# Performance work log

Measured on AMD Instinct MI355X. Metric: run time of the kernel, lower is better.

The kernel has to match this reference:

```python
import jax, jax.numpy as jnp
import numpy as np
import math

B, M, V, C, HID, BIN, H, W = 2, 1024, 300, 128, 128, 256, 384, 512


def fibonacci_sphere(n):
    # generate_grasp_views: n approximately-uniform directions on the unit sphere
    i = np.arange(n, dtype=np.float64)
    phi = (np.sqrt(5.0) - 1.0) / 2.0
    z = (2.0 * i + 1.0) / n - 1.0
    r = np.sqrt(np.maximum(1.0 - z * z, 0.0))
    t = 2.0 * np.pi * i * phi
    v = np.stack([r * np.cos(t), r * np.sin(t), z], -1)
    return (v / np.linalg.norm(v, axis=-1, keepdims=True)).astype(np.float32)


def setup_inputs():
    key = jax.random.key(0)
    ks = jax.random.split(key, 24)
    seed_features = jax.random.normal(ks[0], (B, C, M), jnp.float32)
    token_sel_idx = jax.random.randint(ks[1], (B, M), 0, H * W)
    fx = 525.0
    Kmat = jnp.array([[fx, 0.0, W / 2.0], [0.0, fx, H / 2.0], [0.0, 0.0, 1.0]], jnp.float32)
    K = jnp.broadcast_to(Kmat, (B, 3, 3))
    depth_map = 0.2 + 0.8 * jax.random.uniform(ks[2], (B, 1, H, W), jnp.float32)
    depth_prob = jax.nn.softmax(jax.random.normal(ks[3], (B, BIN, H, W), jnp.float32), axis=1)
    view_dirs = jnp.asarray(fibonacci_sphere(V))

    def lin(k, fan_in, shape):
        s = 1.0 / np.sqrt(fan_in)
        return jax.random.uniform(k, shape, jnp.float32, -s, s)

    qin = C + 7  # seed_feat + ray(3) + normal(3) + uncert(1)
    params = dict(
        Wq1=lin(ks[4], qin, (qin, HID)), bq1=lin(ks[5], qin, (HID,)),
        Wq2=lin(ks[6], HID, (HID, HID)), bq2=lin(ks[7], HID, (HID,)),
        Wa1=lin(ks[8], 3, (3, HID)), ba1=lin(ks[9], 3, (HID,)),
        Wa2=lin(ks[10], HID, (HID, HID)), ba2=lin(ks[11], HID, (HID,)),
        Wb1=lin(ks[12], 3, (3, HID // 2)), bb1=lin(ks[13], 3, (HID // 2,)),
        Wb2=lin(ks[14], HID // 2, (HID // 2, 1)), bb2=lin(ks[15], HID // 2, (1,)),
        Wr1=lin(ks[16], HID, (HID, C)), br1=lin(ks[17], HID, (C,)),
        Wr2=lin(ks[18], C, (C, C)), br2=lin(ks[19], C, (C,)),
    )
    return dict(seed_features=seed_features, token_sel_idx=token_sel_idx, K=K,
                depth_map=depth_map, depth_prob=depth_prob, view_dirs=view_dirs, **params)


def _views_to_rot(views):
    # batch_viewpoint_params_to_matrix(-views, angle=0)
    axis_x = -views
    zero = jnp.zeros_like(axis_x[..., 0])
    axis_y = jnp.stack([-axis_x[..., 1], axis_x[..., 0], zero], -1)
    ny = jnp.linalg.norm(axis_y, axis=-1, keepdims=True)
    fallback = jnp.broadcast_to(jnp.array([0.0, 1.0, 0.0], views.dtype), axis_y.shape)
    axis_y = jnp.where(ny < 1e-8, fallback, axis_y / jnp.maximum(ny, 1e-8))
    axis_x = axis_x / jnp.maximum(jnp.linalg.norm(axis_x, axis=-1, keepdims=True), 1e-8)
    axis_z = jnp.cross(axis_x, axis_y)
    return jnp.stack([axis_x, axis_y, axis_z], -1)  # (B,M,3,3)


def _forward(seed_features, token_sel_idx, K, depth_map, depth_prob, view_dirs,
             Wq1, bq1, Wq2, bq2, Wa1, ba1, Wa2, ba2, Wb1, bb1, Wb2, bb2, Wr1, br1, Wr2, br2):
    depth_map = jax.lax.stop_gradient(depth_map)   # .detach() in torch
    depth_prob = jax.lax.stop_gradient(depth_prob)
    # --- backproject depth to xyz map (B,3,H,W) ---
    ys, xs = jnp.meshgrid(jnp.arange(H, dtype=jnp.float32), jnp.arange(W, dtype=jnp.float32), indexing='ij')
    fx = K[:, 0, 0][:, None, None, None]; fy = K[:, 1, 1][:, None, None, None]
    cx = K[:, 0, 2][:, None, None, None]; cy = K[:, 1, 2][:, None, None, None]
    z = depth_map
    x = (xs[None, None] - cx) / fx * z
    y = (ys[None, None] - cy) / fy * z
    xyz = jnp.concatenate([x, y, z], axis=1)
    # --- central-difference normal map with replicate pad ---
    dx = (xyz[:, :, :, 2:] - xyz[:, :, :, :-2])[:, :, 1:-1, :]
    dy = (xyz[:, :, 2:, :] - xyz[:, :, :-2, :])[:, :, :, 1:-1]
    n = jnp.cross(dx.transpose(0, 2, 3, 1), dy.transpose(0, 2, 3, 1))
    n = n / jnp.maximum(jnp.linalg.norm(n, axis=-1, keepdims=True), 1e-6)
    normal_map = jnp.pad(n.transpose(0, 3, 1, 2), ((0, 0), (0, 0), (1, 1), (1, 1)), mode='edge')
    # --- depth uncertainty: normalized entropy over bins ---
    p = jnp.maximum(depth_prob, 1e-8)
    uncert_map = jnp.clip(-(p * jnp.log(p)).sum(axis=1, keepdims=True) / math.log(BIN), 0.0, 1.0)
    # --- per-seed irregular gathers ---
    def gather(feat, idx):
        Bf, Cf = feat.shape[0], feat.shape[1]
        flat = feat.reshape(Bf, Cf, H * W)
        return jnp.take_along_axis(flat, jnp.broadcast_to(idx[:, None, :], (Bf, Cf, idx.shape[1])), axis=2)
    normal_bm3 = gather(normal_map, token_sel_idx).transpose(0, 2, 1)  # (B,M,3)
    uncert_bm1 = gather(uncert_map, token_sel_idx).transpose(0, 2, 1)  # (B,M,1)
    u = (token_sel_idx % W).astype(jnp.float32)
    v = (token_sel_idx // W).astype(jnp.float32)
    rx = (u - K[:, 0, 2][:, None]) / K[:, 0, 0][:, None]
    ry = (v - K[:, 1, 2][:, None]) / K[:, 1, 1][:, None]
    rays = jnp.stack([rx, ry, jnp.ones_like(rx)], -1)
    rays = rays / jnp.maximum(jnp.linalg.norm(rays, axis=-1, keepdims=True), 1e-12)
    normal_bm3 = normal_bm3 * (1.0 - uncert_bm1)
    # --- query / anchor / bias MLPs ---
    q_in = jnp.concatenate([seed_features.transpose(0, 2, 1), rays, normal_bm3, uncert_bm1], -1)
    q = jax.nn.relu(jax.nn.relu(q_in @ Wq1 + bq1) @ Wq2 + bq2)          # (B,M,HID)
    a = jax.nn.relu(view_dirs @ Wa1 + ba1) @ Wa2 + ba2                  # (V,HID)
    bias = (jax.nn.relu(view_dirs @ Wb1 + bb1) @ Wb2 + bb2)[:, 0]        # (V,)
    logits = jnp.einsum('bmh,vh->bmv', q, a) / jnp.sqrt(jnp.float32(HID)) + bias
    view_score = jax.nn.sigmoid(logits)                                  # (B,M,V)
    # --- top-1 view selection + gather xyz / rot / anchor feat ---
    top_inds = jnp.argmax(view_score, axis=-1)                           # (B,M)
    top_xyz = view_dirs[top_inds]                                        # (B,M,3)
    rot = _views_to_rot(top_xyz)                                         # (B,M,3,3)
    top_a = a[top_inds]                                                  # (B,M,HID)
    res = jax.nn.relu((q + top_a) @ Wr1 + br1) @ Wr2 + br2               # (B,M,C)
    res_feat = res.transpose(0, 2, 1)                                    # (B,C,M)
    return view_score, top_inds, top_xyz, rot, res_feat


def reference(seed_features, token_sel_idx, K, depth_map, depth_prob, view_dirs,
              Wq1, bq1, Wq2, bq2, Wa1, ba1, Wa2, ba2, Wb1, bb1, Wb2, bb2, Wr1, br1, Wr2, br2):
    return _forward(seed_features, token_sel_idx, K, depth_map, depth_prob, view_dirs,
                    Wq1, bq1, Wq2, bq2, Wa1, ba1, Wa2, ba2, Wb1, bb1, Wb2, bb2, Wr1, br1, Wr2, br2)
```

## Files before the change

kernel.cpp:

```cpp
#include <hip/hip_runtime.h>
#include <math.h>

#define B 2
#define M 1024
#define V 300
#define C 128
#define HID 128
#define BIN 256
#define H 384
#define W 512
#define QIN (C + 7)
#define G 4

__global__ __launch_bounds__(HID) void anchor_kernel(
    const float* __restrict__ view_dirs,
    const float* __restrict__ Wa1, const float* __restrict__ ba1,
    const float* __restrict__ Wa2, const float* __restrict__ ba2,
    const float* __restrict__ Wb1, const float* __restrict__ bb1,
    const float* __restrict__ Wb2, const float* __restrict__ bb2,
    float* __restrict__ a_out, float* __restrict__ aT_out,
    float* __restrict__ bias_out) {
  const int v = blockIdx.x;
  const int t = threadIdx.x;
  __shared__ float h1[HID];

  const float vd0 = view_dirs[v * 3 + 0];
  const float vd1 = view_dirs[v * 3 + 1];
  const float vd2 = view_dirs[v * 3 + 2];

  float h = vd0 * Wa1[0 * HID + t] + vd1 * Wa1[1 * HID + t] + vd2 * Wa1[2 * HID + t] + ba1[t];
  h1[t] = fmaxf(h, 0.0f);

  if (t < 64) {
    float x = vd0 * Wb1[0 * 64 + t] + vd1 * Wb1[1 * 64 + t] + vd2 * Wb1[2 * 64 + t] + bb1[t];
    x = fmaxf(x, 0.0f) * Wb2[t];
#pragma unroll
    for (int o = 32; o > 0; o >>= 1) x += __shfl_down(x, o, 64);
    if (t == 0) bias_out[v] = x + bb2[0];
  }
  __syncthreads();

  float acc = ba2[t];
#pragma unroll 8
  for (int k = 0; k < HID; ++k) acc += h1[k] * Wa2[k * HID + t];
  a_out[v * HID + t] = acc;
  aT_out[(size_t)t * V + v] = acc;
}

__global__ __launch_bounds__(128) void seed_kernel(
    const float* __restrict__ seed, const int* __restrict__ token_sel_idx,
    const float* __restrict__ Kmat, const float* __restrict__ depth_map,
    const float* __restrict__ depth_prob, const float* __restrict__ view_dirs,
    const float* __restrict__ Wq1, const float* __restrict__ bq1,
    const float* __restrict__ Wq2, const float* __restrict__ bq2,
    const float* __restrict__ Wr1, const float* __restrict__ br1,
    const float* __restrict__ Wr2, const float* __restrict__ br2,
    const float* __restrict__ a_ws, const float* __restrict__ aT_ws,
    const float* __restrict__ bias_ws,
    float* __restrict__ out_view_score, float* __restrict__ out_top_inds,
    float* __restrict__ out_top_xyz, float* __restrict__ out_rot,
    float* __restrict__ out_res) {
  const int s0 = blockIdx.x * G;
  const int b = s0 >> 10;
  const int m0 = s0 & (M - 1);
  const int t = threadIdx.x;
  const int lane = t & 63;
  const int wv = t >> 6;

  __shared__ __align__(16) float qin_s[G][136];
  __shared__ __align__(16) float hs[G][HID];
  __shared__ __align__(16) float qs[G][HID];
  __shared__ __align__(16) float sum_s[G][HID];
  __shared__ float ered[G][2];
  __shared__ float wbv[G][2];
  __shared__ int   wbi[G][2];
  __shared__ int   sbest[G];
  __shared__ int   sidx[G];

  if (t < G) sidx[t] = token_sel_idx[b * M + m0 + t];

  const float4 sv = *(const float4*)&seed[((size_t)b * C + t) * M + m0];
  __syncthreads();

  float pe[2 * G];
  {
    const size_t HW = (size_t)H * W;
#pragma unroll
    for (int g = 0; g < G; ++g) {
      const float* dp = depth_prob + (size_t)b * BIN * HW + sidx[g];
      pe[2 * g + 0] = dp[(size_t)(2 * t + 0) * HW];
      pe[2 * g + 1] = dp[(size_t)(2 * t + 1) * HW];
    }
  }

  float zl = 0.f, zr = 0.f, zu = 0.f, zd = 0.f;
  int w_r = 0, h_r = 0, wc_r = 0, hc_r = 0;
  if (t < G) {
    const int idx = sidx[t];
    w_r = idx % W;
    h_r = idx / W;
    hc_r = min(max(h_r, 1), H - 2);
    wc_r = min(max(w_r, 1), W - 2);
    const float* dm = depth_map + (size_t)b * H * W;
    zl = dm[hc_r * W + (wc_r - 1)];
    zr = dm[hc_r * W + (wc_r + 1)];
    zu = dm[(hc_r - 1) * W + wc_r];
    zd = dm[(hc_r + 1) * W + wc_r];
  }

  qin_s[0][t] = sv.x; qin_s[1][t] = sv.y; qin_s[2][t] = sv.z; qin_s[3][t] = sv.w;
  if (t < G) qin_s[t][135] = 0.0f;
  __syncthreads();

  float acc[G];
  {
    const float b1 = bq1[t];
#pragma unroll
    for (int g = 0; g < G; ++g) acc[g] = b1;
    for (int i0 = 0; i0 < 128; i0 += 4) {
      const float w0 = Wq1[(i0 + 0) * HID + t];
      const float w1 = Wq1[(i0 + 1) * HID + t];
      const float w2 = Wq1[(i0 + 2) * HID + t];
      const float w3 = Wq1[(i0 + 3) * HID + t];
#pragma unroll
      for (int g = 0; g < G; ++g) {
        const float4 qv = *(const float4*)&qin_s[g][i0];
        acc[g] += qv.x * w0 + qv.y * w1 + qv.z * w2 + qv.w * w3;
      }
    }
  }

  {
    float e[G];
#pragma unroll
    for (int g = 0; g < G; ++g) {
      const float p0 = fmaxf(pe[2 * g + 0], 1e-8f);
      const float p1 = fmaxf(pe[2 * g + 1], 1e-8f);
      e[g] = p0 * logf(p0) + p1 * logf(p1);
    }
#pragma unroll
    for (int o = 32; o > 0; o >>= 1) {
#pragma unroll
      for (int g = 0; g < G; ++g) e[g] += __shfl_down(e[g], o, 64);
    }
    if (lane == 0) {
#pragma unroll
      for (int g = 0; g < G; ++g) ered[g][wv] = e[g];
    }
  }
  __syncthreads();

  if (t < G) {
    const int g = t;
    float uncert = (-(ered[g][0] + ered[g][1])) / 5.5451774444795623f;
    uncert = fminf(fmaxf(uncert, 0.0f), 1.0f);

    const float fx = Kmat[b * 9 + 0], fy = Kmat[b * 9 + 4];
    const float cx = Kmat[b * 9 + 2], cy = Kmat[b * 9 + 5];
    const int w = w_r, h = h_r, hc = hc_r, wc = wc_r;

    const float dxx = (wc + 1 - cx) / fx * zr - (wc - 1 - cx) / fx * zl;
    const float dxy = (hc - cy) / fy * zr - (hc - cy) / fy * zl;
    const float dxz = zr - zl;
    const float dyx = (wc - cx) / fx * zd - (wc - cx) / fx * zu;
    const float dyy = (hc + 1 - cy) / fy * zd - (hc - 1 - cy) / fy * zu;
    const float dyz = zd - zu;

    float nx = dxy * dyz - dxz * dyy;
    float ny = dxz * dyx - dxx * dyz;
    float nz = dxx * dyy - dxy * dyx;
    const float nn = fmaxf(sqrtf(nx * nx + ny * ny + nz * nz), 1e-6f);
    const float sc = (1.0f - uncert) / nn;

    const float rx = ((float)w - cx) / fx;
    const float ry = ((float)h - cy) / fy;
    const float rn = fmaxf(sqrtf(rx * rx + ry * ry + 1.0f), 1e-12f);

    qin_s[g][128] = rx / rn;
    qin_s[g][129] = ry / rn;
    qin_s[g][130] = 1.0f / rn;
    qin_s[g][131] = nx * sc;
    qin_s[g][132] = ny * sc;
    qin_s[g][133] = nz * sc;
    qin_s[g][134] = uncert;
  }
  __syncthreads();

  {
#pragma unroll
    for (int i = 128; i < 135; ++i) {
      const float wv_ = Wq1[i * HID + t];
#pragma unroll
      for (int g = 0; g < G; ++g) acc[g] += qin_s[g][i] * wv_;
    }
#pragma unroll
    for (int g = 0; g < G; ++g) hs[g][t] = fmaxf(acc[g], 0.0f);
  }
  __syncthreads();

  {
    const float b2 = bq2[t];
#pragma unroll
    for (int g = 0; g < G; ++g) acc[g] = b2;
    for (int k0 = 0; k0 < HID; k0 += 4) {
      const float w0 = Wq2[(k0 + 0) * HID + t];
      const float w1 = Wq2[(k0 + 1) * HID + t];
      const float w2 = Wq2[(k0 + 2) * HID + t];
      const float w3 = Wq2[(k0 + 3) * HID + t];
#pragma unroll
      for (int g = 0; g < G; ++g) {
        const float4 hv = *(const float4*)&hs[g][k0];
        acc[g] += hv.x * w0 + hv.y * w1 + hv.z * w2 + hv.w * w3;
      }
    }
#pragma unroll
    for (int g = 0; g < G; ++g) qs[g][t] = fmaxf(acc[g], 0.0f);
  }
  __syncthreads();

  const int col2 = 256 + (t < 44 ? t : 43);
  float d0[G], d1[G], d2[G];
#pragma unroll
  for (int g = 0; g < G; ++g) { d0[g] = 0.0f; d1[g] = 0.0f; d2[g] = 0.0f; }
  for (int k0 = 0; k0 < HID; k0 += 4) {
    const float* r0 = aT_ws + (size_t)(k0 + 0) * V;
    const float* r1 = aT_ws + (size_t)(k0 + 1) * V;
    const float* r2 = aT_ws + (size_t)(k0 + 2) * V;
    const float* r3 = aT_ws + (size_t)(k0 + 3) * V;
    const float a00 = r0[t], a01 = r0[t + 128], a02 = r0[col2];
    const float a10 = r1[t], a11 = r1[t + 128], a12 = r1[col2];
    const float a20 = r2[t], a21 = r2[t + 128], a22 = r2[col2];
    const float a30 = r3[t], a31 = r3[t + 128], a32 = r3[col2];
#pragma unroll
    for (int g = 0; g < G; ++g) {
      const float4 qv = *(const float4*)&qs[g][k0];
      d0[g] += qv.x * a00 + qv.y * a10 + qv.z * a20 + qv.w * a30;
      d1[g] += qv.x * a01 + qv.y * a11 + qv.z * a21 + qv.w * a31;
      d2[g] += qv.x * a02 + qv.y * a12 + qv.z * a22 + qv.w * a32;
    }
  }

  const float rsq = 0.08838834764831845f;
  const float bw0 = bias_ws[t];
  const float bw1 = bias_ws[t + 128];
  const float bw2 = bias_ws[col2];
  float bv[G]; int bi[G];
#pragma unroll
  for (int g = 0; g < G; ++g) {
    const float sc0 = 1.0f / (1.0f + expf(-(d0[g] * rsq + bw0)));
    const float sc1 = 1.0f / (1.0f + expf(-(d1[g] * rsq + bw1)));
    const float sc2 = 1.0f / (1.0f + expf(-(d2[g] * rsq + bw2)));

    float* vs_out = out_view_score + (size_t)(b * M + m0 + g) * V;
    vs_out[t] = sc0;
    vs_out[t + 128] = sc1;
    if (t < 44) vs_out[t + 256] = sc2;

    bv[g] = sc0; bi[g] = t;
    if (sc1 > bv[g]) { bv[g] = sc1; bi[g] = t + 128; }
    if (t < 44 && sc2 > bv[g]) { bv[g] = sc2; bi[g] = t + 256; }
  }
#pragma unroll
  for (int o = 32; o > 0; o >>= 1) {
#pragma unroll
    for (int g = 0; g < G; ++g) {
      const float ov = __shfl_down(bv[g], o, 64);
      const int oi = __shfl_down(bi[g], o, 64);
      if (ov > bv[g] || (ov == bv[g] && oi < bi[g])) { bv[g] = ov; bi[g] = oi; }
    }
  }
  if (lane == 0) {
#pragma unroll
    for (int g = 0; g < G; ++g) { wbv[g][wv] = bv[g]; wbi[g][wv] = bi[g]; }
  }
  __syncthreads();

  if (t < G) {
    const int g = t;
    float fbv = wbv[g][0]; int fbi = wbi[g][0];
    if (wbv[g][1] > fbv || (wbv[g][1] == fbv && wbi[g][1] < fbi)) { fbv = wbv[g][1]; fbi = wbi[g][1]; }
    sbest[g] = fbi;

    const int bm = b * M + m0 + g;
    out_top_inds[bm] = (float)fbi;
    const float vx = view_dirs[fbi * 3 + 0];
    const float vy = view_dirs[fbi * 3 + 1];
    const float vz = view_dirs[fbi * 3 + 2];
    out_top_xyz[(size_t)bm * 3 + 0] = vx;
    out_top_xyz[(size_t)bm * 3 + 1] = vy;
    out_top_xyz[(size_t)bm * 3 + 2] = vz;

    float ax0 = -vx, ax1 = -vy, ax2 = -vz;
    float ay0 = vy, ay1 = -vx, ay2 = 0.0f;
    const float nyn = sqrtf(ay0 * ay0 + ay1 * ay1);
    if (nyn < 1e-8f) {
      ay0 = 0.0f; ay1 = 1.0f; ay2 = 0.0f;
    } else {
      const float d = fmaxf(nyn, 1e-8f);
      ay0 /= d; ay1 /= d;
    }
    const float an = fmaxf(sqrtf(ax0 * ax0 + ax1 * ax1 + ax2 * ax2), 1e-8f);
    ax0 /= an; ax1 /= an; ax2 /= an;
    const float az0 = ax1 * ay2 - ax2 * ay1;
    const float az1 = ax2 * ay0 - ax0 * ay2;
    const float az2 = ax0 * ay1 - ax1 * ay0;
    float* R = out_rot + (size_t)bm * 9;
    R[0] = ax0; R[1] = ay0; R[2] = az0;
    R[3] = ax1; R[4] = ay1; R[5] = az1;
    R[6] = ax2; R[7] = ay2; R[8] = az2;
  }
  __syncthreads();

#pragma unroll
  for (int g = 0; g < G; ++g) sum_s[g][t] = qs[g][t] + a_ws[sbest[g] * HID + t];
  __syncthreads();

  {
    const float b1 = br1[t];
#pragma unroll
    for (int g = 0; g < G; ++g) acc[g] = b1;
    for (int k0 = 0; k0 < HID; k0 += 4) {
      const float w0 = Wr1[(k0 + 0) * HID + t];
      const float w1 = Wr1[(k0 + 1) * HID + t];
      const float w2 = Wr1[(k0 + 2) * HID + t];
      const float w3 = Wr1[(k0 + 3) * HID + t];
#pragma unroll
      for (int g = 0; g < G; ++g) {
        const float4 sv2 = *(const float4*)&sum_s[g][k0];
        acc[g] += sv2.x * w0 + sv2.y * w1 + sv2.z * w2 + sv2.w * w3;
      }
    }
#pragma unroll
    for (int g = 0; g < G; ++g) hs[g][t] = fmaxf(acc[g], 0.0f);
  }
  __syncthreads();

  {
    const float b2 = br2[t];
#pragma unroll
    for (int g = 0; g < G; ++g) acc[g] = b2;
    for (int k0 = 0; k0 < HID; k0 += 4) {
      const float w0 = Wr2[(k0 + 0) * HID + t];
      const float w1 = Wr2[(k0 + 1) * HID + t];
      const float w2 = Wr2[(k0 + 2) * HID + t];
      const float w3 = Wr2[(k0 + 3) * HID + t];
#pragma unroll
      for (int g = 0; g < G; ++g) {
        const float4 hv = *(const float4*)&hs[g][k0];
        acc[g] += hv.x * w0 + hv.y * w1 + hv.z * w2 + hv.w * w3;
      }
    }
    float4 o;
    o.x = acc[0]; o.y = acc[1]; o.z = acc[2]; o.w = acc[3];
    *(float4*)&out_res[((size_t)b * C + t) * M + m0] = o;
  }
}

extern "C" void kernel_launch(void* const* d_in, const int* in_sizes, int n_in,
                              void* d_out, int out_size, void* d_ws, size_t ws_size,
                              hipStream_t stream) {
  const float* seed  = (const float*)d_in[0];
  const int*   tok   = (const int*)d_in[1];
  const float* Km    = (const float*)d_in[2];
  const float* dmap  = (const float*)d_in[3];
  const float* dprob = (const float*)d_in[4];
  const float* vdirs = (const float*)d_in[5];
  const float* Wq1 = (const float*)d_in[6];  const float* bq1 = (const float*)d_in[7];
  const float* Wq2 = (const float*)d_in[8];  const float* bq2 = (const float*)d_in[9];
  const float* Wa1 = (const float*)d_in[10]; const float* ba1 = (const float*)d_in[11];
  const float* Wa2 = (const float*)d_in[12]; const float* ba2 = (const float*)d_in[13];
  const float* Wb1 = (const float*)d_in[14]; const float* bb1 = (const float*)d_in[15];
  const float* Wb2 = (const float*)d_in[16]; const float* bb2 = (const float*)d_in[17];
  const float* Wr1 = (const float*)d_in[18]; const float* br1 = (const float*)d_in[19];
  const float* Wr2 = (const float*)d_in[20]; const float* br2 = (const float*)d_in[21];

  float* out = (float*)d_out;
  float* vs  = out;
  float* ti  = vs + (size_t)B * M * V;
  float* tx  = ti + (size_t)B * M;
  float* rot = tx + (size_t)B * M * 3;
  float* rf  = rot + (size_t)B * M * 9;

  float* a_ws    = (float*)d_ws;
  float* aT_ws   = a_ws + (size_t)V * HID;
  float* bias_ws = aT_ws + (size_t)HID * V;

  anchor_kernel<<<V, HID, 0, stream>>>(vdirs, Wa1, ba1, Wa2, ba2, Wb1, bb1, Wb2, bb2,
                                       a_ws, aT_ws, bias_ws);
  seed_kernel<<<(B * M) / G, 128, 0, stream>>>(seed, tok, Km, dmap, dprob, vdirs,
                                               Wq1, bq1, Wq2, bq2, Wr1, br1, Wr2, br2,
                                               a_ws, aT_ws, bias_ws, vs, ti, tx, rot, rf);
}
```

Baseline: 548.1 us.

## Move per-seed depth entropy and geometry into a widely parallel prep kernel

The scattered depth_prob gathers, entropy reduction, and normal/ray computation move out of the seed MLP kernel into a prep kernel with one 256-thread block per seed point. The same launch also handles the anchor MLP, so the two independent jobs share one launch. The seed kernel then reads a precomputed 8-float tail per seed, folds it into the first matmul loop, and drops two barriers. This spreads the latency-bound strided gathers across many more blocks, at the cost of a small workspace round-trip.

```diff
diff --git a/kernel.cpp b/kernel.cpp
--- a/kernel.cpp
+++ b/kernel.cpp
@@ -12,45 +12,122 @@
 #define QIN (C + 7)
 #define G 4
 
-__global__ __launch_bounds__(HID) void anchor_kernel(
+__global__ __launch_bounds__(256) void prep_kernel(
+    const int* __restrict__ token_sel_idx, const float* __restrict__ Kmat,
+    const float* __restrict__ depth_map, const float* __restrict__ depth_prob,
     const float* __restrict__ view_dirs,
     const float* __restrict__ Wa1, const float* __restrict__ ba1,
     const float* __restrict__ Wa2, const float* __restrict__ ba2,
     const float* __restrict__ Wb1, const float* __restrict__ bb1,
     const float* __restrict__ Wb2, const float* __restrict__ bb2,
     float* __restrict__ a_out, float* __restrict__ aT_out,
-    float* __restrict__ bias_out) {
-  const int v = blockIdx.x;
+    float* __restrict__ bias_out, float* __restrict__ qtail) {
   const int t = threadIdx.x;
-  __shared__ float h1[HID];
-
-  const float vd0 = view_dirs[v * 3 + 0];
-  const float vd1 = view_dirs[v * 3 + 1];
-  const float vd2 = view_dirs[v * 3 + 2];
-
-  float h = vd0 * Wa1[0 * HID + t] + vd1 * Wa1[1 * HID + t] + vd2 * Wa1[2 * HID + t] + ba1[t];
-  h1[t] = fmaxf(h, 0.0f);
-
-  if (t < 64) {
-    float x = vd0 * Wb1[0 * 64 + t] + vd1 * Wb1[1 * 64 + t] + vd2 * Wb1[2 * 64 + t] + bb1[t];
-    x = fmaxf(x, 0.0f) * Wb2[t];
-#pragma unroll
-    for (int o = 32; o > 0; o >>= 1) x += __shfl_down(x, o, 64);
-    if (t == 0) bias_out[v] = x + bb2[0];
-  }
-  __syncthreads();
-
-  float acc = ba2[t];
+
+  if (blockIdx.x < B * M) {
+    const int bm = blockIdx.x;
+    const int b = bm >> 10;
+    const int lane = t & 63;
+    const int wv = t >> 6;
+    __shared__ float ered[4];
+    __shared__ int sidx_s;
+    if (t == 0) sidx_s = token_sel_idx[bm];
+    __syncthreads();
+    const int idx = sidx_s;
+
+    float zl = 0.f, zr = 0.f, zu = 0.f, zd = 0.f;
+    int w_r = 0, h_r = 0, wc_r = 0, hc_r = 0;
+    if (t == 0) {
+      w_r = idx % W;
+      h_r = idx / W;
+      hc_r = min(max(h_r, 1), H - 2);
+      wc_r = min(max(w_r, 1), W - 2);
+      const float* dm = depth_map + (size_t)b * H * W;
+      zl = dm[hc_r * W + (wc_r - 1)];
+      zr = dm[hc_r * W + (wc_r + 1)];
+      zu = dm[(hc_r - 1) * W + wc_r];
+      zd = dm[(hc_r + 1) * W + wc_r];
+    }
+
+    const size_t HW = (size_t)H * W;
+    float p = depth_prob[(size_t)b * BIN * HW + (size_t)t * HW + idx];
+    p = fmaxf(p, 1e-8f);
+    float e = p * logf(p);
+#pragma unroll
+    for (int o = 32; o > 0; o >>= 1) e += __shfl_down(e, o, 64);
+    if (lane == 0) ered[wv] = e;
+    __syncthreads();
+
+    if (t == 0) {
+      float uncert = (-(ered[0] + ered[1] + ered[2] + ered[3])) / 5.5451774444795623f;
+      uncert = fminf(fmaxf(uncert, 0.0f), 1.0f);
+
+      const float fx = Kmat[b * 9 + 0], fy = Kmat[b * 9 + 4];
+      const float cx = Kmat[b * 9 + 2], cy = Kmat[b * 9 + 5];
+      const int w = w_r, h = h_r, hc = hc_r, wc = wc_r;
+
+      const float dxx = (wc + 1 - cx) / fx * zr - (wc - 1 - cx) / fx * zl;
+      const float dxy = (hc - cy) / fy * zr - (hc - cy) / fy * zl;
+      const float dxz = zr - zl;
+      const float dyx = (wc - cx) / fx * zd - (wc - cx) / fx * zu;
+      const float dyy = (hc + 1 - cy) / fy * zd - (hc - 1 - cy) / fy * zu;
+      const float dyz = zd - zu;
+
+      float nx = dxy * dyz - dxz * dyy;
+      float ny = dxz * dyx - dxx * dyz;
+      float nz = dxx * dyy - dxy * dyx;
+      const float nn = fmaxf(sqrtf(nx * nx + ny * ny + nz * nz), 1e-6f);
+      const float sc = (1.0f - uncert) / nn;
+
+      const float rx = ((float)w - cx) / fx;
+      const float ry = ((float)h - cy) / fy;
+      const float rn = fmaxf(sqrtf(rx * rx + ry * ry + 1.0f), 1e-12f);
+
+      float* q = qtail + (size_t)bm * 8;
+      q[0] = rx / rn;
+      q[1] = ry / rn;
+      q[2] = 1.0f / rn;
+      q[3] = nx * sc;
+      q[4] = ny * sc;
+      q[5] = nz * sc;
+      q[6] = uncert;
+      q[7] = 0.0f;
+    }
+  } else {
+    const int v = blockIdx.x - B * M;
+    __shared__ float h1[HID];
+
+    if (t < HID) {
+      const float vd0 = view_dirs[v * 3 + 0];
+      const float vd1 = view_dirs[v * 3 + 1];
+      const float vd2 = view_dirs[v * 3 + 2];
+
+      float h = vd0 * Wa1[0 * HID + t] + vd1 * Wa1[1 * HID + t] + vd2 * Wa1[2 * HID + t] + ba1[t];
+      h1[t] = fmaxf(h, 0.0f);
+
+      if (t < 64) {
+        float x = vd0 * Wb1[0 * 64 + t] + vd1 * Wb1[1 * 64 + t] + vd2 * Wb1[2 * 64 + t] + bb1[t];
+        x = fmaxf(x, 0.0f) * Wb2[t];
+#pragma unroll
+        for (int o = 32; o > 0; o >>= 1) x += __shfl_down(x, o, 64);
+        if (t == 0) bias_out[v] = x + bb2[0];
+      }
+    }
+    __syncthreads();
+
+    if (t < HID) {
+      float acc = ba2[t];
 #pragma unroll 8
-  for (int k = 0; k < HID; ++k) acc += h1[k] * Wa2[k * HID + t];
-  a_out[v * HID + t] = acc;
-  aT_out[(size_t)t * V + v] = acc;
+      for (int k = 0; k < HID; ++k) acc += h1[k] * Wa2[k * HID + t];
+      a_out[v * HID + t] = acc;
+      aT_out[(size_t)t * V + v] = acc;
+    }
+  }
 }
 
 __global__ __launch_bounds__(128) void seed_kernel(
-    const float* __restrict__ seed, const int* __restrict__ token_sel_idx,
-    const float* __restrict__ Kmat, const float* __restrict__ depth_map,
-    const float* __restrict__ depth_prob, const float* __restrict__ view_dirs,
+    const float* __restrict__ seed, const float* __restrict__ qtail,
+    const float* __restrict__ view_dirs,
     const float* __restrict__ Wq1, const float* __restrict__ bq1,
     const float* __restrict__ Wq2, const float* __restrict__ bq2,
     const float* __restrict__ Wr1, const float* __restrict__ br1,
@@ -71,45 +148,17 @@
   __shared__ __align__(16) float hs[G][HID];
   __shared__ __align__(16) float qs[G][HID];
   __shared__ __align__(16) float sum_s[G][HID];
-  __shared__ float ered[G][2];
   __shared__ float wbv[G][2];
   __shared__ int   wbi[G][2];
   __shared__ int   sbest[G];
-  __shared__ int   sidx[G];
-
-  if (t < G) sidx[t] = token_sel_idx[b * M + m0 + t];
 
   const float4 sv = *(const float4*)&seed[((size_t)b * C + t) * M + m0];
-  __syncthreads();
-
-  float pe[2 * G];
-  {
-    const size_t HW = (size_t)H * W;
-#pragma unroll
-    for (int g = 0; g < G; ++g) {
-      const float* dp = depth_prob + (size_t)b * BIN * HW + sidx[g];
-      pe[2 * g + 0] = dp[(size_t)(2 * t + 0) * HW];
-      pe[2 * g + 1] = dp[(size_t)(2 * t + 1) * HW];
-    }
-  }
-
-  float zl = 0.f, zr = 0.f, zu = 0.f, zd = 0.f;
-  int w_r = 0, h_r = 0, wc_r = 0, hc_r = 0;
-  if (t < G) {
-    const int idx = sidx[t];
-    w_r = idx % W;
-    h_r = idx / W;
-    hc_r = min(max(h_r, 1), H - 2);
-    wc_r = min(max(w_r, 1), W - 2);
-    const float* dm = depth_map + (size_t)b * H * W;
-    zl = dm[hc_r * W + (wc_r - 1)];
-    zr = dm[hc_r * W + (wc_r + 1)];
-    zu = dm[(hc_r - 1) * W + wc_r];
-    zd = dm[(hc_r + 1) * W + wc_r];
-  }
-
+  if (t < 2 * G) {
+    const int g = t >> 1, half = t & 1;
+    ((float4*)&qin_s[g][128])[half] =
+        ((const float4*)(qtail + (size_t)(s0 + g) * 8))[half];
+  }
   qin_s[0][t] = sv.x; qin_s[1][t] = sv.y; qin_s[2][t] = sv.z; qin_s[3][t] = sv.w;
-  if (t < G) qin_s[t][135] = 0.0f;
   __syncthreads();
 
   float acc[G];
@@ -117,7 +166,7 @@
     const float b1 = bq1[t];
 #pragma unroll
     for (int g = 0; g < G; ++g) acc[g] = b1;
-    for (int i0 = 0; i0 < 128; i0 += 4) {
+    for (int i0 = 0; i0 < 132; i0 += 4) {
       const float w0 = Wq1[(i0 + 0) * HID + t];
       const float w1 = Wq1[(i0 + 1) * HID + t];
       const float w2 = Wq1[(i0 + 2) * HID + t];
@@ -128,70 +177,15 @@
         acc[g] += qv.x * w0 + qv.y * w1 + qv.z * w2 + qv.w * w3;
       }
     }
-  }
-
-  {
-    float e[G];
-#pragma unroll
-    for (int g = 0; g < G; ++g) {
-      const float p0 = fmaxf(pe[2 * g + 0], 1e-8f);
-      const float p1 = fmaxf(pe[2 * g + 1], 1e-8f);
-      e[g] = p0 * logf(p0) + p1 * logf(p1);
-    }
-#pragma unroll
-    for (int o = 32; o > 0; o >>= 1) {
-#pragma unroll
-      for (int g = 0; g < G; ++g) e[g] += __shfl_down(e[g], o, 64);
-    }
-    if (lane == 0) {
-#pragma unroll
-      for (int g = 0; g < G; ++g) ered[g][wv] = e[g];
-    }
-  }
-  __syncthreads();
-
-  if (t < G) {
-    const int g = t;
-    float uncert = (-(ered[g][0] + ered[g][1])) / 5.5451774444795623f;
-    uncert = fminf(fmaxf(uncert, 0.0f), 1.0f);
-
-    const float fx = Kmat[b * 9 + 0], fy = Kmat[b * 9 + 4];
-    const float cx = Kmat[b * 9 + 2], cy = Kmat[b * 9 + 5];
-    const int w = w_r, h = h_r, hc = hc_r, wc = wc_r;
-
-    const float dxx = (wc + 1 - cx) / fx * zr - (wc - 1 - cx) / fx * zl;
-    const float dxy = (hc - cy) / fy * zr - (hc - cy) / fy * zl;
-    const float dxz = zr - zl;
-    const float dyx = (wc - cx) / fx * zd - (wc - cx) / fx * zu;
-    const float dyy = (hc + 1 - cy) / fy * zd - (hc - 1 - cy) / fy * zu;
-    const float dyz = zd - zu;
-
-    float nx = dxy * dyz - dxz * dyy;
-    float ny = dxz * dyx - dxx * dyz;
-    float nz = dxx * dyy - dxy * dyx;
-    const float nn = fmaxf(sqrtf(nx * nx + ny * ny + nz * nz), 1e-6f);
-    const float sc = (1.0f - uncert) / nn;
-
-    const float rx = ((float)w - cx) / fx;
-    const float ry = ((float)h - cy) / fy;
-    const float rn = fmaxf(sqrtf(rx * rx + ry * ry + 1.0f), 1e-12f);
-
-    qin_s[g][128] = rx / rn;
-    qin_s[g][129] = ry / rn;
-    qin_s[g][130] = 1.0f / rn;
-    qin_s[g][131] = nx * sc;
-    qin_s[g][132] = ny * sc;
-    qin_s[g][133] = nz * sc;
-    qin_s[g][134] = uncert;
-  }
-  __syncthreads();
-
-  {
-#pragma unroll
-    for (int i = 128; i < 135; ++i) {
-      const float wv_ = Wq1[i * HID + t];
-#pragma unroll
-      for (int g = 0; g < G; ++g) acc[g] += qin_s[g][i] * wv_;
+    {
+      const float w0 = Wq1[132 * HID + t];
+      const float w1 = Wq1[133 * HID + t];
+      const float w2 = Wq1[134 * HID + t];
+#pragma unroll
+      for (int g = 0; g < G; ++g) {
+        const float4 qv = *(const float4*)&qin_s[g][132];
+        acc[g] += qv.x * w0 + qv.y * w1 + qv.z * w2;
+      }
     }
 #pragma unroll
     for (int g = 0; g < G; ++g) hs[g][t] = fmaxf(acc[g], 0.0f);
@@ -251,7 +245,7 @@
     const float sc1 = 1.0f / (1.0f + expf(-(d1[g] * rsq + bw1)));
     const float sc2 = 1.0f / (1.0f + expf(-(d2[g] * rsq + bw2)));
 
-    float* vs_out = out_view_score + (size_t)(b * M + m0 + g) * V;
+    float* vs_out = out_view_score + (size_t)(s0 + g) * V;
     vs_out[t] = sc0;
     vs_out[t + 128] = sc1;
     if (t < 44) vs_out[t + 256] = sc2;
@@ -281,7 +275,7 @@
     if (wbv[g][1] > fbv || (wbv[g][1] == fbv && wbi[g][1] < fbi)) { fbv = wbv[g][1]; fbi = wbi[g][1]; }
     sbest[g] = fbi;
 
-    const int bm = b * M + m0 + g;
+    const int bm = s0 + g;
     out_top_inds[bm] = (float)fbi;
     const float vx = view_dirs[fbi * 3 + 0];
     const float vy = view_dirs[fbi * 3 + 1];
@@ -384,10 +378,12 @@
   float* a_ws    = (float*)d_ws;
   float* aT_ws   = a_ws + (size_t)V * HID;
   float* bias_ws = aT_ws + (size_t)HID * V;
-
-  anchor_kernel<<<V, HID, 0, stream>>>(vdirs, Wa1, ba1, Wa2, ba2, Wb1, bb1, Wb2, bb2,
-                                       a_ws, aT_ws, bias_ws);
-  seed_kernel<<<(B * M) / G, 128, 0, stream>>>(seed, tok, Km, dmap, dprob, vdirs,
+  float* qtail   = bias_ws + V;
+
+  prep_kernel<<<B * M + V, 256, 0, stream>>>(tok, Km, dmap, dprob, vdirs,
+                                             Wa1, ba1, Wa2, ba2, Wb1, bb1, Wb2, bb2,
+                                             a_ws, aT_ws, bias_ws, qtail);
+  seed_kernel<<<(B * M) / G, 128, 0, stream>>>(seed, qtail, vdirs,
                                                Wq1, bq1, Wq2, bq2, Wr1, br1, Wr2, br2,
                                                a_ws, aT_ws, bias_ws, vs, ti, tx, rot, rf);
 }
```

New measurement: 544.0 us. No clear change (-0.8%).
